# Optimization experiments

Hardware: AMD Instinct MI355X
Metric: run time of the kernel (lower is better)

## Reference

```python
import jax, jax.numpy as jnp
import numpy as np

NUM_HEADS = 16


def _local_attn(q, k, v, bias, nq, nk):
    """Blocked local attention, faithful to rearrange_to_dense_trunk semantics.
    q,k,v: [B,H,N,D]; bias: [B,Hb,N,N] (Hb broadcasts against H).
    Trunk i (queries [i*nq,(i+1)*nq)) attends keys at original indices
    [i*nq - pad_left, i*nq - pad_left + nk); out-of-range keys/values/bias are
    zero-padded (the module pads with zeros, no -inf key masking).
    Assumes N % nq == 0 (q_pad_length == 0, so the query mask loop is a no-op).
    """
    B, H, N, D = q.shape
    T = N // nq                      # n_trunks
    pad_left = (nk - nq) // 2
    Lp = (T - 1) * nq + nk           # padded key length so every window is full
    pad_right = Lp - pad_left - N
    k_p = jnp.pad(k, ((0, 0), (0, 0), (pad_left, pad_right), (0, 0)))
    v_p = jnp.pad(v, ((0, 0), (0, 0), (pad_left, pad_right), (0, 0)))
    b_p = jnp.pad(bias, ((0, 0), (0, 0), (0, 0), (pad_left, pad_right)))
    # window gather indices: [T, nk]
    kidx = jnp.arange(T)[:, None] * nq + jnp.arange(nk)[None, :]
    k_t = k_p[:, :, kidx, :]         # [B,H,T,nk,D]
    v_t = v_p[:, :, kidx, :]         # [B,H,T,nk,D]
    Bb, Hb = bias.shape[0], bias.shape[1]
    b_r = b_p.reshape(Bb, Hb, T, nq, Lp)
    b_t = jnp.take_along_axis(b_r, kidx[None, None, :, None, :], axis=-1)  # [Bb,Hb,T,nq,nk]
    q_t = q.reshape(B, H, T, nq, D)
    scores = jnp.einsum('bhtqd,bhtkd->bhtqk', q_t, k_t) + b_t
    w = jax.nn.softmax(scores, axis=-1)
    o = jnp.einsum('bhtqk,bhtkd->bhtqd', w, v_t)
    return o.reshape(B, H, N, D)


def setup_inputs() -> dict:
    key = jax.random.key(0)
    ks = jax.random.split(key, 8)
    B, N, C = 1, 4096, 256
    H, D = NUM_HEADS, 64
    HD = H * D
    q_x = jax.random.normal(ks[0], (B, N, C), dtype=jnp.float32)
    kv_x = jax.random.normal(ks[1], (B, N, C), dtype=jnp.float32)
    attn_bias = jax.random.normal(ks[2], (B, 1, N, N), dtype=jnp.float32) * 0.1
    Wq = jax.random.normal(ks[3], (C, HD), dtype=jnp.float32) / np.sqrt(C).astype(np.float32)
    Wk = jax.random.normal(ks[4], (C, HD), dtype=jnp.float32) / np.sqrt(C).astype(np.float32)
    Wv = jax.random.normal(ks[5], (C, HD), dtype=jnp.float32) / np.sqrt(C).astype(np.float32)
    Wg = jax.random.normal(ks[6], (C, HD), dtype=jnp.float32) / np.sqrt(C).astype(np.float32)
    Wo = jax.random.normal(ks[7], (HD, C), dtype=jnp.float32) / np.sqrt(HD).astype(np.float32)
    return {"q_x": q_x, "kv_x": kv_x, "attn_bias": attn_bias,
            "Wq": Wq, "Wk": Wk, "Wv": Wv, "Wg": Wg, "Wo": Wo,
            "n_queries": 64, "n_keys": 256}


def reference(q_x, kv_x, attn_bias, Wq, Wk, Wv, Wg, Wo, n_queries, n_keys):
    B, N, C = q_x.shape
    H = NUM_HEADS
    D = Wq.shape[-1] // H
    def split_heads(x):
        return x.reshape(B, N, H, D).transpose(0, 2, 1, 3)  # [B,H,N,D]
    q = split_heads(q_x @ Wq) / jnp.sqrt(jnp.float32(D))
    k = split_heads(kv_x @ Wk)
    v = split_heads(kv_x @ Wv)
    o = _local_attn(q, k, v, attn_bias, n_queries, n_keys)
    o = o.transpose(0, 2, 1, 3).reshape(B, N, H * D)
    g = jax.nn.sigmoid(q_x @ Wg)  # gating head
    return (o * g) @ Wo
```

## Files before the change

### kernel.cpp

```cpp
#include <hip/hip_runtime.h>

#define N_ 4096
#define C_ 256
#define H_ 16
#define D_ 64
#define HD_ 1024

typedef __attribute__((ext_vector_type(8))) _Float16 f16x8;
typedef __attribute__((ext_vector_type(4))) _Float16 f16x4;
typedef __attribute__((ext_vector_type(4))) float f32x4;

__device__ __forceinline__ void gload16(const void* g, void* l) {
    __builtin_amdgcn_global_load_lds(
        (const __attribute__((address_space(1))) unsigned int*)g,
        (__attribute__((address_space(3))) unsigned int*)l, 16, 0, 0);
}

__global__ __launch_bounds__(256) void convert_kernel(
    const float* __restrict__ q_x, const float* __restrict__ kv_x,
    const float* __restrict__ Wq, const float* __restrict__ Wk,
    const float* __restrict__ Wv, const float* __restrict__ Wg,
    const float* __restrict__ Wo,
    _Float16* __restrict__ Xf, _Float16* __restrict__ WTf,
    _Float16* __restrict__ WoTf)
{
    __shared__ float ts[64][65];
    const int b = blockIdx.x;
    const int tid = threadIdx.x;

    if (b < 512) {
        const int seg = b >> 8;
        const float* src = seg ? kv_x : q_x;
        _Float16* df = Xf + (size_t)seg * 1048576;
        const int base = (b & 255) * 4096 + tid * 16;
#pragma unroll
        for (int q = 0; q < 4; ++q) {
            float4 v = *(const float4*)&src[base + q * 4];
            f16x4 fv;
            fv[0] = (_Float16)v.x; fv[1] = (_Float16)v.y;
            fv[2] = (_Float16)v.z; fv[3] = (_Float16)v.w;
            *(f16x4*)&df[base + q * 4] = fv;
        }
        return;
    }

    const float* src;
    _Float16* df;
    int srcC, dstC, r0, c0;
    if (b < 768) {
        const int widx = (b - 512) >> 6;
        const int tile = (b - 512) & 63;
        src = (widx == 0) ? Wq : (widx == 1) ? Wk : (widx == 2) ? Wv : Wg;
        df = WTf + (size_t)widx * 262144;
        srcC = 1024; dstC = 256;
        r0 = (tile >> 4) * 64;
        c0 = (tile & 15) * 64;
    } else {
        const int tile = b - 768;
        src = Wo; df = WoTf;
        srcC = 256; dstC = 1024;
        r0 = (tile >> 2) * 64;
        c0 = (tile & 3) * 64;
    }
    {
        const int r = tid >> 2;
        const int cch = (tid & 3) * 16;
#pragma unroll
        for (int q = 0; q < 4; ++q) {
            float4 v = *(const float4*)&src[(size_t)(r0 + r) * srcC + c0 + cch + q * 4];
            ts[r][cch + q * 4 + 0] = v.x;
            ts[r][cch + q * 4 + 1] = v.y;
            ts[r][cch + q * 4 + 2] = v.z;
            ts[r][cch + q * 4 + 3] = v.w;
        }
    }
    __syncthreads();
    {
        const int c = tid >> 2;
        const int rch = (tid & 3) * 16;
#pragma unroll
        for (int q = 0; q < 4; ++q) {
            f16x4 fv;
#pragma unroll
            for (int j = 0; j < 4; ++j)
                fv[j] = (_Float16)ts[rch + q * 4 + j][c];
            *(f16x4*)&df[(size_t)(c0 + c) * dstC + r0 + rch + q * 4] = fv;
        }
    }
}

__global__ __launch_bounds__(256) void proj_mfma(
    const _Float16* __restrict__ Xf, const _Float16* __restrict__ WTf,
    _Float16* __restrict__ qh, _Float16* __restrict__ kh,
    _Float16* __restrict__ vh, _Float16* __restrict__ gh)
{
    __shared__ __align__(16) char psmem[34816];
    _Float16* As = (_Float16*)psmem;
    _Float16* Bs = (_Float16*)(psmem + 16384);

    const int lb  = blockIdx.x;
    const int xcd = lb & 7;
    const int gr  = (lb >> 6) * 8 + xcd;
    const int g   = gr >> 5;
    const int m0  = (gr & 31) * 128;
    const int c0  = ((lb >> 3) & 7) * 128;

    const _Float16* A = Xf + ((g == 1 || g == 2) ? 1048576 : 0);
    const _Float16* B = WTf + (size_t)g * 262144;

    const int tid  = threadIdx.x;
    const int wave = tid >> 6;
    const int lane = tid & 63;
    const int wr   = wave >> 1;
    const int wc   = wave & 1;
    const int frow = lane & 15;
    const int grp  = lane >> 4;

    f32x4 acc[4][4];
#pragma unroll
    for (int i = 0; i < 4; ++i)
#pragma unroll
        for (int j = 0; j < 4; ++j) acc[i][j] = (f32x4){0.f, 0.f, 0.f, 0.f};

    const int srow = tid >> 3;
    const int sch  = tid & 7;

    for (int kt = 0; kt < 256; kt += 64) {
        __syncthreads();
#pragma unroll
        for (int p = 0; p < 4; ++p) {
            const int row = p * 32 + srow;
            const int koff = kt + ((sch ^ (row & 7)) << 3);
            gload16(A + (size_t)(m0 + row) * 256 + koff, (char*)As + p * 4096 + tid * 16);
            gload16(B + (size_t)(c0 + row) * 256 + koff, (char*)Bs + p * 4096 + tid * 16);
        }
        __syncthreads();

#pragma unroll
        for (int ks = 0; ks < 2; ++ks) {
            f16x8 af[4], bf[4];
#pragma unroll
            for (int f = 0; f < 4; ++f) {
                const int ra = wr * 64 + f * 16 + frow;
                const int rb = wc * 64 + f * 16 + frow;
                af[f] = *(const f16x8*)((char*)As + ra * 128 + (((ks * 4 + grp) ^ (ra & 7)) << 4));
                bf[f] = *(const f16x8*)((char*)Bs + rb * 128 + (((ks * 4 + grp) ^ (rb & 7)) << 4));
            }
#pragma unroll
            for (int i = 0; i < 4; ++i)
#pragma unroll
                for (int j = 0; j < 4; ++j)
                    acc[i][j] = __builtin_amdgcn_mfma_f32_16x16x32_f16(af[i], bf[j], acc[i][j], 0, 0, 0);
        }
    }

    __syncthreads();
    _Float16* Epi = (_Float16*)psmem;
    {
        const float scale = (g == 0) ? 0.125f : 1.f;
#pragma unroll
        for (int i = 0; i < 4; ++i)
#pragma unroll
            for (int j = 0; j < 4; ++j) {
                const int rr = wr * 64 + i * 16 + grp * 4;
                const int cc = wc * 64 + j * 16 + frow;
#pragma unroll
                for (int v = 0; v < 4; ++v) {
                    float x = acc[i][j][v];
                    x = (g == 3) ? 1.f / (1.f + __expf(-x)) : x * scale;
                    Epi[(rr + v) * 136 + cc] = (_Float16)x;
                }
            }
    }
    __syncthreads();
    {
        const int ch   = tid & 15;
        const int head = ch >> 3;
        const int e8   = (ch & 7) * 8;
#pragma unroll
        for (int p = 0; p < 8; ++p) {
            const int r = p * 16 + (tid >> 4);
            const f16x8 val = *(const f16x8*)&Epi[r * 136 + head * 64 + e8];
            if (g == 3) {
                *(f16x8*)&gh[(size_t)(m0 + r) * HD_ + c0 + head * 64 + e8] = val;
            } else {
                _Float16* dst = (g == 0) ? qh : (g == 1) ? kh : vh;
                const int hh = (c0 >> 6) + head;
                *(f16x8*)&dst[((size_t)hh * N_ + m0 + r) * D_ + e8] = val;
            }
        }
    }
}

__global__ __launch_bounds__(256, 4) void attn_mfma(
    const _Float16* __restrict__ qh, const _Float16* __restrict__ kh,
    const _Float16* __restrict__ vh, const float* __restrict__ bias,
    const _Float16* __restrict__ gh, _Float16* __restrict__ of)
{
    __shared__ __align__(16) char smem[40960];
    _Float16* Qs = (_Float16*)smem;
    char* Ks = smem + 8192;
    _Float16* Ps = (_Float16*)smem;
    _Float16* Vs = (_Float16*)(smem + 17408);
    float* Oe = (float*)smem;

    const int lb  = blockIdx.x;
    const int xcd = lb & 7;
    const int j_  = lb >> 3;
    const int h   = j_ >> 3;
    const int t   = xcd * 8 + (j_ & 7);
    const int tid = threadIdx.x;
    const int lane = tid & 63;
    const int wv = tid >> 6;
    const int frow = lane & 15;
    const int grp = lane >> 4;
    const int kbase = t * 64 - 96;

    const char* qbase = (const char*)qh + (size_t)(h * N_ + t * 64) * 128;
    const char* kbase_p = (const char*)kh + (size_t)h * N_ * 128;

#pragma unroll
    for (int q = 0; q < 2; ++q) {
        const int lin = q * 4096 + tid * 16;
        const int row = lin >> 7;
        const int ch = (lin >> 4) & 7;
        gload16(qbase + row * 128 + ((ch ^ (row & 7)) << 4), (char*)Qs + lin);
    }
#pragma unroll
    for (int q = 0; q < 8; ++q) {
        const int lin = q * 4096 + tid * 16;
        const int row = lin >> 7;
        const int ch = (lin >> 4) & 7;
        const int kg = kbase + row;
        if ((unsigned)kg < (unsigned)N_) {
            gload16(kbase_p + (size_t)kg * 128 + ((ch ^ (row & 7)) << 4), Ks + lin);
        } else {
            *(float4*)(Ks + lin) = make_float4(0.f, 0.f, 0.f, 0.f);
        }
    }

    f32x4 sacc[16];
    {
        const int rowg = t * 64 + wv * 16 + grp * 4;
#pragma unroll
        for (int j = 0; j < 16; ++j) {
            const int colg = kbase + j * 16 + frow;
            const bool ok = (unsigned)colg < (unsigned)N_;
#pragma unroll
            for (int v = 0; v < 4; ++v)
                sacc[j][v] = ok ? bias[(size_t)(rowg + v) * N_ + colg] : 0.f;
        }
    }
    __syncthreads();

    {
        const int rq = wv * 16 + frow;
#pragma unroll
        for (int ks = 0; ks < 2; ++ks) {
            const f16x8 aq = *(const f16x8*)((char*)Qs + rq * 128 + (((ks * 4 + grp) ^ (rq & 7)) << 4));
#pragma unroll
            for (int j = 0; j < 16; ++j) {
                const int rk = j * 16 + frow;
                const f16x8 bk = *(const f16x8*)(Ks + rk * 128 + (((ks * 4 + grp) ^ (rk & 7)) << 4));
                sacc[j] = __builtin_amdgcn_mfma_f32_16x16x32_f16(aq, bk, sacc[j], 0, 0, 0);
            }
        }
    }
    __syncthreads();

    float inv[4];
#pragma unroll
    for (int v = 0; v < 4; ++v) {
        float m = sacc[0][v];
#pragma unroll
        for (int f = 1; f < 16; ++f) m = fmaxf(m, sacc[f][v]);
        m = fmaxf(m, __shfl_xor(m, 1));
        m = fmaxf(m, __shfl_xor(m, 2));
        m = fmaxf(m, __shfl_xor(m, 4));
        m = fmaxf(m, __shfl_xor(m, 8));
        float l = 0.f;
#pragma unroll
        for (int f = 0; f < 16; ++f) {
            float e = __expf(sacc[f][v] - m);
            sacc[f][v] = e;
            l += e;
        }
        l += __shfl_xor(l, 1);
        l += __shfl_xor(l, 2);
        l += __shfl_xor(l, 4);
        l += __shfl_xor(l, 8);
        inv[v] = 1.f / l;
    }

    f32x4 oacc[4];
#pragma unroll
    for (int jd = 0; jd < 4; ++jd) oacc[jd] = (f32x4){0.f, 0.f, 0.f, 0.f};

#pragma unroll
    for (int c = 0; c < 2; ++c) {
        {
            const int sl = tid >> 1;
            const int d0 = (tid & 1) * 32;
            const int kg = kbase + c * 128 + sl;
            f16x8 vv[4];
            if ((unsigned)kg < (unsigned)N_) {
                const f16x8* vp = (const f16x8*)(vh + ((size_t)h * N_ + kg) * D_ + d0);
#pragma unroll
                for (int q = 0; q < 4; ++q) vv[q] = vp[q];
            } else {
#pragma unroll
                for (int q = 0; q < 4; ++q)
#pragma unroll
                    for (int e = 0; e < 8; ++e) vv[q][e] = (_Float16)0.f;
            }
#pragma unroll
            for (int q = 0; q < 4; ++q)
#pragma unroll
                for (int e = 0; e < 8; ++e)
                    Vs[(d0 + q * 8 + e) * 136 + sl] = vv[q][e];
        }
        {
            const int rb = wv * 16 + grp * 4;
#pragma unroll
            for (int j = 0; j < 8; ++j) {
                const int col = j * 16 + frow;
#pragma unroll
                for (int v = 0; v < 4; ++v)
                    Ps[(rb + v) * 136 + col] = (_Float16)sacc[c * 8 + j][v];
            }
        }
        __syncthreads();
        const int rp = wv * 16 + frow;
#pragma unroll
        for (int ks = 0; ks < 4; ++ks) {
            const f16x8 ap = *(const f16x8*)((char*)Ps + rp * 272 + ks * 64 + grp * 16);
#pragma unroll
            for (int jd = 0; jd < 4; ++jd) {
                const f16x8 bv = *(const f16x8*)((char*)Vs + (jd * 16 + frow) * 272 + ks * 64 + grp * 16);
                oacc[jd] = __builtin_amdgcn_mfma_f32_16x16x32_f16(ap, bv, oacc[jd], 0, 0, 0);
            }
        }
        __syncthreads();
    }

#pragma unroll
    for (int jd = 0; jd < 4; ++jd) {
        const int dcol = jd * 16 + frow;
#pragma unroll
        for (int v = 0; v < 4; ++v) {
            const int rn = wv * 16 + grp * 4 + v;
            Oe[rn * 68 + dcol] = oacc[jd][v] * inv[v];
        }
    }
    __syncthreads();
    {
        const int r   = tid >> 2;
        const int seg = tid & 3;
        const int n   = t * 64 + r;
        const int cg0 = h * 64 + seg * 16;
        const float* orow = &Oe[r * 68 + seg * 16];
        f32x4 o0 = *(const f32x4*)&orow[0];
        f32x4 o1 = *(const f32x4*)&orow[4];
        f32x4 o2 = *(const f32x4*)&orow[8];
        f32x4 o3 = *(const f32x4*)&orow[12];
        const f16x8 g0 = *(const f16x8*)&gh[(size_t)n * HD_ + cg0];
        const f16x8 g1 = *(const f16x8*)&gh[(size_t)n * HD_ + cg0 + 8];
        f16x8 r0, r1;
#pragma unroll
        for (int e = 0; e < 4; ++e) {
            r0[e]     = (_Float16)(o0[e] * (float)g0[e]);
            r0[4 + e] = (_Float16)(o1[e] * (float)g0[4 + e]);
            r1[e]     = (_Float16)(o2[e] * (float)g1[e]);
            r1[4 + e] = (_Float16)(o3[e] * (float)g1[4 + e]);
        }
        *(f16x8*)&of[(size_t)n * HD_ + cg0]     = r0;
        *(f16x8*)&of[(size_t)n * HD_ + cg0 + 8] = r1;
    }
}

__global__ __launch_bounds__(256) void out_mfma(
    const _Float16* __restrict__ of, const _Float16* __restrict__ WoTf,
    float* __restrict__ out)
{
    __shared__ __align__(16) _Float16 smem[2048 + 4096];
    _Float16* As = smem;
    _Float16* Bs = smem + 2048;

    const int lb  = blockIdx.x;
    const int xcd = lb & 7;
    const int s   = lb >> 3;
    const int rowt = (s >> 2) * 8 + xcd;
    const int m0  = rowt * 32;
    const int c0  = (s & 3) * 64;

    const int tid  = threadIdx.x;
    const int wave = tid >> 6;
    const int lane = tid & 63;
    const int wr   = wave >> 1;
    const int wc   = wave & 1;
    const int frow = lane & 15;
    const int grp  = lane >> 4;

    f32x4 acc[2];
#pragma unroll
    for (int j = 0; j < 2; ++j) acc[j] = (f32x4){0.f, 0.f, 0.f, 0.f};

    for (int kt = 0; kt < 1024; kt += 64) {
        __syncthreads();
        {
            const int row = tid >> 3;
            const int ch  = tid & 7;
            const int koff = kt + ((ch ^ (row & 7)) << 3);
            gload16(of + (size_t)(m0 + row) * HD_ + koff, (char*)As + tid * 16);
        }
#pragma unroll
        for (int p = 0; p < 2; ++p) {
            const int lin = p * 4096 + tid * 16;
            const int row = lin >> 7;
            const int ch  = (lin >> 4) & 7;
            const int koff = kt + ((ch ^ (row & 7)) << 3);
            gload16(WoTf + (size_t)(c0 + row) * HD_ + koff, (char*)Bs + lin);
        }
        __syncthreads();

#pragma unroll
        for (int ks = 0; ks < 2; ++ks) {
            const int ra = wr * 16 + frow;
            const f16x8 af = *(const f16x8*)((char*)As + ra * 128 + (((ks * 4 + grp) ^ (ra & 7)) << 4));
#pragma unroll
            for (int j = 0; j < 2; ++j) {
                const int rb = wc * 32 + j * 16 + frow;
                const f16x8 bf = *(const f16x8*)((char*)Bs + rb * 128 + (((ks * 4 + grp) ^ (rb & 7)) << 4));
                acc[j] = __builtin_amdgcn_mfma_f32_16x16x32_f16(af, bf, acc[j], 0, 0, 0);
            }
        }
    }

    const int rbase = grp * 4;
#pragma unroll
    for (int j = 0; j < 2; ++j) {
        const int c = c0 + wc * 32 + j * 16 + frow;
#pragma unroll
        for (int v = 0; v < 4; ++v) {
            const int n = m0 + wr * 16 + rbase + v;
            out[(size_t)n * C_ + c] = acc[j][v];
        }
    }
}

extern "C" void kernel_launch(void* const* d_in, const int* in_sizes, int n_in,
                              void* d_out, int out_size, void* d_ws, size_t ws_size,
                              hipStream_t stream)
{
    const float* q_x  = (const float*)d_in[0];
    const float* kv_x = (const float*)d_in[1];
    const float* bias = (const float*)d_in[2];
    const float* Wq   = (const float*)d_in[3];
    const float* Wk   = (const float*)d_in[4];
    const float* Wv   = (const float*)d_in[5];
    const float* Wg   = (const float*)d_in[6];
    const float* Wo   = (const float*)d_in[7];
    float* out = (float*)d_out;

    char* ws = (char*)d_ws;
    const size_t MB = 1048576;
    _Float16* qh   = (_Float16*)(ws);
    _Float16* kh   = (_Float16*)(ws + 8  * MB);
    _Float16* vh   = (_Float16*)(ws + 16 * MB);
    _Float16* gh   = (_Float16*)(ws + 24 * MB);
    _Float16* of   = (_Float16*)(ws + 32 * MB);
    _Float16* Xf   = (_Float16*)(ws + 40 * MB);
    _Float16* WTf  = (_Float16*)(ws + 44 * MB);
    _Float16* WoTf = (_Float16*)(ws + 46 * MB);

    convert_kernel<<<832, 256, 0, stream>>>(q_x, kv_x, Wq, Wk, Wv, Wg, Wo,
                                            Xf, WTf, WoTf);
    proj_mfma<<<1024, 256, 0, stream>>>(Xf, WTf, qh, kh, vh, gh);
    attn_mfma<<<1024, 256, 0, stream>>>(qh, kh, vh, bias, gh, of);
    out_mfma<<<512, 256, 0, stream>>>(of, WoTf, out);
}
```

Measured before the change: 161.2 us.

## Store V transposed in projection and stream it via async LDS loads

The projection kernel now writes V directly in a [head*D, N] transposed layout from the accumulators, skipping the LDS epilogue for that group. The attention kernel fetches V tiles with global_load_lds into a swizzled LDS layout and zeroes out-of-range keys only for boundary trunks. This replaces the per-element scalar LDS transpose of V. The softmax is moved after the first V load is issued so the load overlaps the exp work, and P uses a matching XOR swizzle. The projection's V stores become strided 8-byte writes, which may coalesce poorly.

Measured after the change: 162.3 us. Within noise of the previous version (+0.7%).

```diff
diff --git a/kernel.cpp b/kernel.cpp
--- a/kernel.cpp
+++ b/kernel.cpp
@@ -92,7 +92,7 @@
 __global__ __launch_bounds__(256) void proj_mfma(
     const _Float16* __restrict__ Xf, const _Float16* __restrict__ WTf,
     _Float16* __restrict__ qh, _Float16* __restrict__ kh,
-    _Float16* __restrict__ vh, _Float16* __restrict__ gh)
+    _Float16* __restrict__ vt, _Float16* __restrict__ gh)
 {
     __shared__ __align__(16) char psmem[34816];
     _Float16* As = (_Float16*)psmem;
@@ -154,6 +154,21 @@
         }
     }
 
+    if (g == 2) {
+#pragma unroll
+        for (int i = 0; i < 4; ++i)
+#pragma unroll
+            for (int j = 0; j < 4; ++j) {
+                const int dglob = c0 + wc * 64 + j * 16 + frow;
+                const int n = m0 + wr * 64 + i * 16 + grp * 4;
+                f16x4 pv;
+#pragma unroll
+                for (int v = 0; v < 4; ++v) pv[v] = (_Float16)acc[i][j][v];
+                *(f16x4*)&vt[((size_t)dglob << 12) + n] = pv;
+            }
+        return;
+    }
+
     __syncthreads();
     _Float16* Epi = (_Float16*)psmem;
     {
@@ -184,7 +199,7 @@
             if (g == 3) {
                 *(f16x8*)&gh[(size_t)(m0 + r) * HD_ + c0 + head * 64 + e8] = val;
             } else {
-                _Float16* dst = (g == 0) ? qh : (g == 1) ? kh : vh;
+                _Float16* dst = (g == 0) ? qh : kh;
                 const int hh = (c0 >> 6) + head;
                 *(f16x8*)&dst[((size_t)hh * N_ + m0 + r) * D_ + e8] = val;
             }
@@ -194,14 +209,14 @@
 
 __global__ __launch_bounds__(256, 4) void attn_mfma(
     const _Float16* __restrict__ qh, const _Float16* __restrict__ kh,
-    const _Float16* __restrict__ vh, const float* __restrict__ bias,
+    const _Float16* __restrict__ vt, const float* __restrict__ bias,
     const _Float16* __restrict__ gh, _Float16* __restrict__ of)
 {
     __shared__ __align__(16) char smem[40960];
     _Float16* Qs = (_Float16*)smem;
     char* Ks = smem + 8192;
-    _Float16* Ps = (_Float16*)smem;
-    _Float16* Vs = (_Float16*)(smem + 17408);
+    char* Ps = smem;
+    char* Vs = smem + 16384;
     float* Oe = (float*)smem;
 
     const int lb  = blockIdx.x;
@@ -269,74 +284,83 @@
     __syncthreads();
 
     float inv[4];
-#pragma unroll
-    for (int v = 0; v < 4; ++v) {
-        float m = sacc[0][v];
-#pragma unroll
-        for (int f = 1; f < 16; ++f) m = fmaxf(m, sacc[f][v]);
-        m = fmaxf(m, __shfl_xor(m, 1));
-        m = fmaxf(m, __shfl_xor(m, 2));
-        m = fmaxf(m, __shfl_xor(m, 4));
-        m = fmaxf(m, __shfl_xor(m, 8));
-        float l = 0.f;
-#pragma unroll
-        for (int f = 0; f < 16; ++f) {
-            float e = __expf(sacc[f][v] - m);
-            sacc[f][v] = e;
-            l += e;
-        }
-        l += __shfl_xor(l, 1);
-        l += __shfl_xor(l, 2);
-        l += __shfl_xor(l, 4);
-        l += __shfl_xor(l, 8);
-        inv[v] = 1.f / l;
-    }
-
     f32x4 oacc[4];
 #pragma unroll
     for (int jd = 0; jd < 4; ++jd) oacc[jd] = (f32x4){0.f, 0.f, 0.f, 0.f};
 
 #pragma unroll
     for (int c = 0; c < 2; ++c) {
+        const int cb = kbase + c * 128;
+        const bool bnd = (c == 0) ? (t <= 1) : (t >= 62);
         {
-            const int sl = tid >> 1;
-            const int d0 = (tid & 1) * 32;
-            const int kg = kbase + c * 128 + sl;
-            f16x8 vv[4];
-            if ((unsigned)kg < (unsigned)N_) {
-                const f16x8* vp = (const f16x8*)(vh + ((size_t)h * N_ + kg) * D_ + d0);
-#pragma unroll
-                for (int q = 0; q < 4; ++q) vv[q] = vp[q];
-            } else {
-#pragma unroll
-                for (int q = 0; q < 4; ++q)
-#pragma unroll
-                    for (int e = 0; e < 8; ++e) vv[q][e] = (_Float16)0.f;
-            }
-#pragma unroll
-            for (int q = 0; q < 4; ++q)
-#pragma unroll
-                for (int e = 0; e < 8; ++e)
-                    Vs[(d0 + q * 8 + e) * 136 + sl] = vv[q][e];
+#pragma unroll
+            for (int q = 0; q < 4; ++q) {
+                const int lin = q * 4096 + tid * 16;
+                const int d  = lin >> 8;
+                const int cs = (lin >> 4) & 15;
+                const int cl = (cs & 8) | ((cs & 7) ^ (d & 7));
+                const int kg0 = cb + cl * 8;
+                const int kgc = kg0 < 0 ? 0 : (kg0 > N_ - 8 ? N_ - 8 : kg0);
+                gload16(vt + (((size_t)(h * 64 + d)) << 12) + kgc, Vs + lin);
+            }
+        }
+        if (c == 0) {
+#pragma unroll
+            for (int v = 0; v < 4; ++v) {
+                float m = sacc[0][v];
+#pragma unroll
+                for (int f = 1; f < 16; ++f) m = fmaxf(m, sacc[f][v]);
+                m = fmaxf(m, __shfl_xor(m, 1));
+                m = fmaxf(m, __shfl_xor(m, 2));
+                m = fmaxf(m, __shfl_xor(m, 4));
+                m = fmaxf(m, __shfl_xor(m, 8));
+                float l = 0.f;
+#pragma unroll
+                for (int f = 0; f < 16; ++f) {
+                    float e = __expf(sacc[f][v] - m);
+                    sacc[f][v] = e;
+                    l += e;
+                }
+                l += __shfl_xor(l, 1);
+                l += __shfl_xor(l, 2);
+                l += __shfl_xor(l, 4);
+                l += __shfl_xor(l, 8);
+                inv[v] = 1.f / l;
+            }
         }
         {
-            const int rb = wv * 16 + grp * 4;
 #pragma unroll
             for (int j = 0; j < 8; ++j) {
-                const int col = j * 16 + frow;
-#pragma unroll
-                for (int v = 0; v < 4; ++v)
-                    Ps[(rb + v) * 136 + col] = (_Float16)sacc[c * 8 + j][v];
+#pragma unroll
+                for (int v = 0; v < 4; ++v) {
+                    const int r = wv * 16 + grp * 4 + v;
+                    const int byt = r * 256 + ((j * 32 + frow * 2) ^ ((r & 7) << 4));
+                    *(_Float16*)(Ps + byt) = (_Float16)sacc[c * 8 + j][v];
+                }
             }
         }
         __syncthreads();
+        if (bnd) {
+#pragma unroll
+            for (int q = 0; q < 4; ++q) {
+                const int lin = q * 4096 + tid * 16;
+                const int d  = lin >> 8;
+                const int cs = (lin >> 4) & 15;
+                const int cl = (cs & 8) | ((cs & 7) ^ (d & 7));
+                const int kg0 = cb + cl * 8;
+                if ((unsigned)kg0 >= (unsigned)N_)
+                    *(float4*)(Vs + lin) = make_float4(0.f, 0.f, 0.f, 0.f);
+            }
+            __syncthreads();
+        }
         const int rp = wv * 16 + frow;
 #pragma unroll
         for (int ks = 0; ks < 4; ++ks) {
-            const f16x8 ap = *(const f16x8*)((char*)Ps + rp * 272 + ks * 64 + grp * 16);
+            const f16x8 ap = *(const f16x8*)(Ps + rp * 256 + (((ks * 4 + grp) ^ (rp & 7)) << 4));
 #pragma unroll
             for (int jd = 0; jd < 4; ++jd) {
-                const f16x8 bv = *(const f16x8*)((char*)Vs + (jd * 16 + frow) * 272 + ks * 64 + grp * 16);
+                const int rd = jd * 16 + frow;
+                const f16x8 bv = *(const f16x8*)(Vs + rd * 256 + (((ks * 4 + grp) ^ (rd & 7)) << 4));
                 oacc[jd] = __builtin_amdgcn_mfma_f32_16x16x32_f16(ap, bv, oacc[jd], 0, 0, 0);
             }
         }
@@ -466,7 +490,7 @@
     const size_t MB = 1048576;
     _Float16* qh   = (_Float16*)(ws);
     _Float16* kh   = (_Float16*)(ws + 8  * MB);
-    _Float16* vh   = (_Float16*)(ws + 16 * MB);
+    _Float16* vt   = (_Float16*)(ws + 16 * MB);
     _Float16* gh   = (_Float16*)(ws + 24 * MB);
     _Float16* of   = (_Float16*)(ws + 32 * MB);
     _Float16* Xf   = (_Float16*)(ws + 40 * MB);
@@ -475,7 +499,7 @@
 
     convert_kernel<<<832, 256, 0, stream>>>(q_x, kv_x, Wq, Wk, Wv, Wg, Wo,
                                             Xf, WTf, WoTf);
-    proj_mfma<<<1024, 256, 0, stream>>>(Xf, WTf, qh, kh, vh, gh);
-    attn_mfma<<<1024, 256, 0, stream>>>(qh, kh, vh, bias, gh, of);
+    proj_mfma<<<1024, 256, 0, stream>>>(Xf, WTf, qh, kh, vt, gh);
+    attn_mfma<<<1024, 256, 0, stream>>>(qh, kh, vt, bias, gh, of);
     out_mfma<<<512, 256, 0, stream>>>(of, WoTf, out);
 }
```
